# Kernel optimization log

Hardware: AMD Instinct MI355X
Metric: run time of the kernel (lower is better)

Reference implementation:

```python
import jax, jax.numpy as jnp
import numpy as np

MODE = 'max'  # matches init kwarg `mode`
EPS = 1e-6

def before_after(x):
    n, d = x.shape
    zero = jnp.zeros((1, d), dtype=x.dtype)
    if MODE == 'max':
        # exclusive prefix max (x_before[0] = 0, matching torch.zeros_like base)
        pre = jax.lax.cummax(x, axis=0)
        before = jnp.concatenate([zero, pre[:-1]], axis=0)
        suf = jax.lax.cummax(x[::-1], axis=0)[::-1]
        after = jnp.concatenate([suf[1:], zero], axis=0)
    else:  # mean
        cs = jnp.cumsum(x, axis=0)
        cnt_b = jnp.arange(1, n, dtype=x.dtype)[:, None]
        before = jnp.concatenate([zero, cs[:-1] / cnt_b], axis=0)
        total = cs[-1]
        cnt_a = jnp.arange(n - 1, 0, -1, dtype=x.dtype)[:, None]
        after = jnp.concatenate([(total[None, :] - cs[:-1]) / cnt_a, zero], axis=0)
    return before, after

def setup_inputs() -> dict:
    key = jax.random.key(0)
    ks = jax.random.split(key, 6)
    n, dim, dff = 8192, 1024, 4096
    s1 = 1.0 / np.sqrt(3 * dim)
    s2 = 1.0 / np.sqrt(dff)
    return {
        'x': jax.random.normal(ks[0], (n, dim), jnp.float32),
        'W1': jax.random.normal(ks[1], (dff, 3 * dim), jnp.float32) * s1,
        'b1': jax.random.normal(ks[2], (dff,), jnp.float32) * s1,
        'ln_w': jnp.ones((dff,), jnp.float32),
        'ln_b': jnp.zeros((dff,), jnp.float32),
        'W2': jax.random.normal(ks[3], (dim, dff), jnp.float32) * s2,
        'b2': jax.random.normal(ks[4], (dim,), jnp.float32) * s2,
        'gamma': jnp.full((dim,), 1e-6, jnp.float32),
    }

def reference(x, W1, b1, ln_w, ln_b, W2, b2, gamma):
    shortcut = x
    before, after = before_after(x)
    h = jnp.concatenate([x, before, after], axis=1)          # [n, 3*dim]
    h = jax.nn.relu(h @ W1.T + b1)                           # [n, dff]
    mu = jnp.mean(h, axis=-1, keepdims=True)
    var = jnp.mean(jnp.square(h - mu), axis=-1, keepdims=True)
    h = (h - mu) * jax.lax.rsqrt(var + EPS) * ln_w + ln_b
    # dropout is identity in eval mode
    out = h @ W2.T + b2                                      # [n, dim]
    return out * gamma[None, :] + shortcut
```

## Files before the change

kernel.cpp:

```cpp
#include <hip/hip_runtime.h>

typedef __attribute__((ext_vector_type(4))) float f32x4;
typedef __attribute__((ext_vector_type(8))) short s16x8;
typedef __attribute__((ext_vector_type(8))) unsigned short u16x8;

#define AS1(p) ((const __attribute__((address_space(1))) void*)(p))
#define AS3(p) ((__attribute__((address_space(3))) void*)(p))

__device__ __forceinline__ unsigned short f2bf(float f) {
  unsigned u = __builtin_bit_cast(unsigned, f);
  u += 0x7fffu + ((u >> 16) & 1u);
  return (unsigned short)(u >> 16);
}
__device__ __forceinline__ float bf2f(unsigned short s) {
  unsigned u = ((unsigned)s) << 16;
  return __builtin_bit_cast(float, u);
}
__device__ __forceinline__ unsigned f2e4m3(float f) {
  unsigned uf = __builtin_bit_cast(unsigned, f);
  unsigned s = (uf >> 24) & 0x80u;
  unsigned u = uf & 0x7fffffffu;
  if (u < 0x3c800000u) return s;
  if (u > 0x43e00000u) u = 0x43e00000u;
  u += 0x7ffffu + ((u >> 20) & 1u);
  unsigned v = (u >> 20) - 960u;
  if (v > 126u) v = 126u;
  return s | v;
}


__global__ __launch_bounds__(256) void cast_weights(const float* __restrict__ W1,
                                                    unsigned char* __restrict__ W1q,
                                                    long n1,
                                                    const float* __restrict__ W2,
                                                    unsigned short* __restrict__ W2b,
                                                    long n2) {
  if (blockIdx.x < 1536) {
    long i = ((long)blockIdx.x * 256 + threadIdx.x) * 4;
    long stride = (long)1536 * 256 * 4;
    for (; i < n1; i += stride) {
      float4 f = *(const float4*)(W1 + i);
      unsigned v = f2e4m3(f.x * 32.f) | (f2e4m3(f.y * 32.f) << 8) |
                   (f2e4m3(f.z * 32.f) << 16) | (f2e4m3(f.w * 32.f) << 24);
      long n = i / 3072;
      long k = i - n * 3072;
      long phys = n * 3072 + (k & ~(long)127) + ((k & 127) ^ ((n & 15) << 3));
      *(unsigned*)(W1q + phys) = v;
    }
  } else {
    long i = ((long)(blockIdx.x - 1536) * 256 + threadIdx.x) * 4;
    long stride = (long)512 * 256 * 4;
    for (; i < n2; i += stride) {
      float4 f = *(const float4*)(W2 + i);
      ushort4 o = { f2bf(f.x), f2bf(f.y), f2bf(f.z), f2bf(f.w) };
      *(ushort4*)(W2b + i) = o;
    }
  }
}

__global__ __launch_bounds__(256) void w2_fold(const float* __restrict__ W2,
                                               const float* __restrict__ lnw,
                                               const float* __restrict__ lnb,
                                               float* __restrict__ w2l,
                                               float* __restrict__ b2l) {
  const int n = blockIdx.x;
  const float* w = W2 + (long)n * 4096;
  float s = 0.f, b = 0.f;
  for (int k = threadIdx.x; k < 4096; k += 256) {
    float wv = w[k];
    s += wv * lnw[k];
    b += wv * lnb[k];
  }
#pragma unroll
  for (int off = 32; off; off >>= 1) {
    s += __shfl_xor(s, off, 64);
    b += __shfl_xor(b, off, 64);
  }
  __shared__ float ss[4], bb[4];
  const int wv2 = threadIdx.x >> 6;
  if ((threadIdx.x & 63) == 0) { ss[wv2] = s; bb[wv2] = b; }
  __syncthreads();
  if (threadIdx.x == 0) {
    w2l[n] = ss[0] + ss[1] + ss[2] + ss[3];
    b2l[n] = bb[0] + bb[1] + bb[2] + bb[3];
  }
}

__global__ __launch_bounds__(256) void scan_chunkmax(const float* __restrict__ x,
                                                     float* __restrict__ partial) {
  int col = blockIdx.x * 256 + threadIdx.x;
  int chunk = blockIdx.y;
  const float* p = x + (long)chunk * 64 * 1024 + col;
  float m = -INFINITY;
#pragma unroll 4
  for (int i = 0; i < 64; i++) m = fmaxf(m, p[(long)i * 1024]);
  partial[chunk * 1024 + col] = m;
}

__global__ __launch_bounds__(256) void scan_chunkscan(const float* __restrict__ partial,
                                                      float* __restrict__ prefix,
                                                      float* __restrict__ suffix) {
  int col = blockIdx.x * 256 + threadIdx.x;
  float v[128];
#pragma unroll
  for (int c = 0; c < 128; c++) v[c] = partial[c * 1024 + col];
  float run = -INFINITY;
#pragma unroll
  for (int c = 0; c < 128; c++) {
    prefix[c * 1024 + col] = run;
    run = fmaxf(run, v[c]);
  }
  run = -INFINITY;
#pragma unroll
  for (int c = 127; c >= 0; c--) {
    suffix[c * 1024 + col] = run;
    run = fmaxf(run, v[c]);
  }
}

__global__ __launch_bounds__(256) void scan_emit(const float* __restrict__ x,
                                                 const float* __restrict__ prefix,
                                                 const float* __restrict__ suffix,
                                                 unsigned char* __restrict__ h_in) {
  int col = blockIdx.x * 256 + threadIdx.x;
  int chunk = blockIdx.y;
  long r0 = (long)chunk * 64;
  const int cb = col & ~127, cw = col & 127;
  float run = prefix[chunk * 1024 + col];
  for (int i = 0; i < 64; i++) {
    long row = r0 + i;
    int xo = (int)(row & 15) << 3;
    int c0 = cb | (cw ^ xo);
    float v = x[row * 1024 + col];
    unsigned char* hr = h_in + row * 3072;
    hr[c0] = (unsigned char)f2e4m3(v);
    hr[1024 + c0] = (unsigned char)(row == 0 ? 0u : f2e4m3(run));
    run = fmaxf(run, v);
  }
  float run2 = suffix[chunk * 1024 + col];
  for (int i = 63; i >= 0; i--) {
    long row = r0 + i;
    int xo = (int)(row & 15) << 3;
    int c0 = cb | (cw ^ xo);
    float v = x[row * 1024 + col];
    h_in[row * 3072 + 2048 + c0] = (unsigned char)(row == 8191 ? 0u : f2e4m3(run2));
    run2 = fmaxf(run2, v);
  }
}

__global__ __launch_bounds__(256) void ln_stats_reduce(const float* __restrict__ pp,
                                                       float* __restrict__ rowstats) {
  int row = blockIdx.x * 256 + threadIdx.x;
  int tm = row >> 8, rl = row & 255;
  float s = 0.f, q = 0.f;
#pragma unroll
  for (int tn = 0; tn < 16; ++tn) {
    const float* p = pp + (((long)(tm * 16 + tn) * 256 + rl) * 2);
    s += p[0];
    q += p[1];
  }
  float mu = s * (1.f / 4096.f);
  float var = q * (1.f / 4096.f) - mu * mu;
  rowstats[row * 2] = mu;
  rowstats[row * 2 + 1] = rsqrtf(var + 1e-6f);
}

__global__ __launch_bounds__(512, 2) void gemm256_relu(
    const unsigned char* __restrict__ A, const unsigned char* __restrict__ B,
    unsigned short* __restrict__ C, const float* __restrict__ bias,
    const float* __restrict__ lnw, float* __restrict__ pp,
    int M, int N, int K) {
  extern __shared__ char smem[];
  const int NT = K >> 7;

  const int nwg = gridDim.x;
  const int cpx = nwg >> 3;
  const int bid = blockIdx.x;
  const int swz = (bid & 7) * cpx + (bid >> 3);
  const int tiles_m = M >> 8;
  const int tm = swz % tiles_m;
  const int tn = swz / tiles_m;
  const long brow = (long)tm * 256;
  const long bcol = (long)tn * 256;

  const int t = threadIdx.x;
  const int lane = t & 63, wv = t >> 6;
  const int wr = wv >> 2, wc = wv & 3;
  const int fr = lane & 15, fk = lane >> 4;

  const int srow = t >> 3;
  const int scol = (t & 7) * 16;
  const unsigned char* Asrc = A + (brow + srow) * (long)K + scol;
  const unsigned char* Bsrc = B + (bcol + srow) * (long)K + scol;
  const long hstep = (long)128 * K, lstep = (long)64 * K;

#define STAGE_A(j, reg, h, L)                                                   \
  __builtin_amdgcn_global_load_lds(AS1(Asrc + (h)*hstep + (L)*lstep + (j)*128), \
      AS3(smem + (reg)*32768 + (h)*16384 + (L)*8192 + t * 16), 16, 0, 0)
#define STAGE_B(j, h, L)                                                        \
  __builtin_amdgcn_global_load_lds(AS1(Bsrc + (h)*hstep + (L)*lstep + (j)*128), \
      AS3(smem + 98304 + ((j)&1) * 32768 + (h)*16384 + (L)*8192 + t * 16), 16, 0, 0)

  const int xr = fr << 3;
  const char* ArdRow = smem + (wr * 128 + fr) * 128;
  const char* BrdRow = smem + 98304 + (wc * 64 + fr) * 128;
#define RD_A(ar_, m, kk) \
  (*(const long*)(ArdRow + (ar_)*32768 + (m)*2048 + (((kk)*32 + fk * 8) ^ xr)))
#define RD_B(pb_, n, kk) \
  (*(const long*)(BrdRow + (pb_)*32768 + (n)*2048 + (((kk)*32 + fk * 8) ^ xr)))

#define MFMA_QUAD(mi, a_)                                                      \
  _Pragma("unroll")                                                            \
  for (int n = 0; n < 4; ++n) {                                                \
    _Pragma("unroll")                                                          \
    for (int kk = 0; kk < 4; ++kk)                                             \
      acc[(mi)][n] = __builtin_amdgcn_mfma_f32_16x16x32_fp8_fp8(               \
          a_[kk], bfr[n][kk], acc[(mi)][n], 0, 0, 0);                          \
  }

  f32x4 acc[8][4];
#pragma unroll
  for (int m = 0; m < 8; m++)
#pragma unroll
    for (int n = 0; n < 4; n++) acc[m][n] = (f32x4)0.f;

  STAGE_A(0, 0, 0, 0); STAGE_A(0, 0, 0, 1); STAGE_A(0, 0, 1, 0); STAGE_A(0, 0, 1, 1);
  STAGE_B(0, 0, 0); STAGE_B(0, 0, 1); STAGE_B(0, 1, 0); STAGE_B(0, 1, 1);
  STAGE_A(1, 1, 0, 0); STAGE_A(1, 1, 0, 1); STAGE_A(1, 1, 1, 0); STAGE_A(1, 1, 1, 1);
  STAGE_B(1, 0, 0); STAGE_B(1, 0, 1); STAGE_B(1, 1, 0); STAGE_B(1, 1, 1);
  asm volatile("s_waitcnt vmcnt(8)" ::: "memory");
  __builtin_amdgcn_s_barrier();

  long bfr[4][4];
  long ap[2][2][4];
  ap[0][0][0] = RD_A(0, 0, 0); ap[0][0][1] = RD_A(0, 0, 1);
  ap[0][0][2] = RD_A(0, 0, 2); ap[0][0][3] = RD_A(0, 0, 3);
  ap[0][1][0] = RD_A(0, 1, 0); ap[0][1][1] = RD_A(0, 1, 1);
  ap[0][1][2] = RD_A(0, 1, 2); ap[0][1][3] = RD_A(0, 1, 3);

  int ar = 0;
  for (int g = 0; g < NT; ++g) {
    const int pb = g & 1;
    int sr = ar + 2; if (sr >= 3) sr -= 3;
    int nar = ar + 1; if (nar >= 3) nar = 0;
    const bool st = (g + 2 < NT);
#pragma unroll
    for (int p = 0; p < 4; ++p) {
      const int cs = p & 1, ns = cs ^ 1;
      if (p == 0) {
#pragma unroll
        for (int n = 0; n < 4; ++n)
#pragma unroll
          for (int kk = 0; kk < 4; ++kk) bfr[n][kk] = RD_B(pb, n, kk);
      }
      asm volatile("s_waitcnt lgkmcnt(0)" ::: "memory");
      __builtin_amdgcn_sched_barrier(0);
      __builtin_amdgcn_s_setprio(1);
      MFMA_QUAD(2 * p, ap[cs][0])
      MFMA_QUAD(2 * p + 1, ap[cs][1])
      __builtin_amdgcn_s_setprio(0);
      if (p < 3) {
#pragma unroll
        for (int kk = 0; kk < 4; ++kk) {
          ap[ns][0][kk] = RD_A(ar, 2 * p + 2, kk);
          ap[ns][1][kk] = RD_A(ar, 2 * p + 3, kk);
        }
      } else if (g + 1 < NT) {
#pragma unroll
        for (int kk = 0; kk < 4; ++kk) {
          ap[ns][0][kk] = RD_A(nar, 0, kk);
          ap[ns][1][kk] = RD_A(nar, 1, kk);
        }
      }
      if (st) {
        if (p == 0) { STAGE_A(g + 2, sr, 0, 0); STAGE_A(g + 2, sr, 0, 1); }
        if (p == 1) { STAGE_A(g + 2, sr, 1, 0); STAGE_A(g + 2, sr, 1, 1); }
        if (p == 2) { STAGE_B(g + 2, 0, 0); STAGE_B(g + 2, 0, 1); }
        if (p == 3) { STAGE_B(g + 2, 1, 0); STAGE_B(g + 2, 1, 1); }
      }
      if (p == 2 && g + 1 < NT) {
        if (st) asm volatile("s_waitcnt vmcnt(6)" ::: "memory");
        else    asm volatile("s_waitcnt vmcnt(0)" ::: "memory");
      }
      asm volatile("s_barrier" ::: "memory");
    }
    ar = nar;
  }

  float bi[4], lw[4];
#pragma unroll
  for (int n = 0; n < 4; ++n) {
    const long col = bcol + wc * 64 + n * 16 + fr;
    bi[n] = bias[col];
    lw[n] = lnw[col];
  }
  float* sred = (float*)smem;
  float* qred = sred + 1024;
  const long orow = brow + wr * 128 + fk * 4;
  const long ocol = bcol + wc * 64 + fr;
#pragma unroll
  for (int m = 0; m < 8; ++m) {
#pragma unroll
    for (int r = 0; r < 4; ++r) {
      const long row = orow + m * 16 + r;
      float s = 0.f, q = 0.f;
#pragma unroll
      for (int n = 0; n < 4; ++n) {
        float v = acc[m][n][r] * 0.03125f + bi[n];
        v = v > 0.f ? v : 0.f;
        s += v;
        q += v * v;
        C[row * (long)N + ocol + n * 16] = f2bf(v * lw[n]);
      }
#pragma unroll
      for (int off = 1; off < 16; off <<= 1) {
        s += __shfl_xor(s, off, 64);
        q += __shfl_xor(q, off, 64);
      }
      if (fr == 0) {
        int rl = wr * 128 + m * 16 + fk * 4 + r;
        sred[rl * 4 + wc] = s;
        qred[rl * 4 + wc] = q;
      }
    }
  }
  __syncthreads();
  if (t < 256) {
    float s = sred[t * 4] + sred[t * 4 + 1] + sred[t * 4 + 2] + sred[t * 4 + 3];
    float q = qred[t * 4] + qred[t * 4 + 1] + qred[t * 4 + 2] + qred[t * 4 + 3];
    float* pb = pp + (((long)(tm * 16 + tn) * 256 + t) * 2);
    pb[0] = s;
    pb[1] = q;
  }
#undef STAGE_A
#undef STAGE_B
#undef RD_A
#undef RD_B
#undef MFMA_QUAD
}

__global__ __launch_bounds__(512, 2) void gemm256_g2(
    const unsigned short* __restrict__ A, const unsigned short* __restrict__ B,
    float* __restrict__ Cf, const float* __restrict__ bias,
    const float* __restrict__ gamma, const float* __restrict__ resid,
    const float* __restrict__ w2l, const float* __restrict__ b2l,
    const float* __restrict__ rowstats,
    int M, int N, int K) {
  extern __shared__ char smem[];
  const int NT = K >> 6;

  const int nwg = gridDim.x;
  const int cpx = nwg >> 3;
  const int bid = blockIdx.x;
  const int swz = (bid & 7) * cpx + (bid >> 3);
  const int tiles_m = M >> 8;
  const int tm = swz % tiles_m;
  const int tn = swz / tiles_m;
  const long brow = (long)tm * 256;
  const long bcol = (long)tn * 128;

  const int t = threadIdx.x;
  const int lane = t & 63, wv = t >> 6;
  const int wr = wv >> 1, wc = wv & 1;
  const int fr = lane & 15, fk = lane >> 4;

  const int srow = t >> 3;
  const int scol = 8 * ((t & 7) ^ ((t >> 3) & 7));
  const unsigned short* Asrc = A + (brow + srow) * (long)K + scol;
  const unsigned short* Bsrc = B + (bcol + srow) * (long)K + scol;
  const long hstep = (long)128 * K, lstep = (long)64 * K;

#define STAGE_A2(j, reg, h, L)                                                 \
  __builtin_amdgcn_global_load_lds(AS1(Asrc + (h)*hstep + (L)*lstep + (j)*64), \
      AS3(smem + (reg)*32768 + (h)*16384 + (L)*8192 + t * 16), 16, 0, 0)
#define STAGE_B2(j, L)                                                         \
  __builtin_amdgcn_global_load_lds(AS1(Bsrc + (L)*lstep + (j)*64),             \
      AS3(smem + 98304 + ((j)&1) * 16384 + (L)*8192 + t * 16), 16, 0, 0)

  const int xr = (fr & 7) << 4;
  const char* ArdRow = smem + (wr * 64 + fr) * 128;
  const char* BrdRow = smem + 98304 + (wc * 64 + fr) * 128;
#define RD_A2(ar_, m, kk) \
  (*(const s16x8*)(ArdRow + (ar_)*32768 + (m)*2048 + (((kk)*64 + fk * 16) ^ xr)))
#define RD_B2(pb_, n, kk) \
  (*(const s16x8*)(BrdRow + (pb_)*16384 + (n)*2048 + (((kk)*64 + fk * 16) ^ xr)))

  f32x4 acc[4][4];
#pragma unroll
  for (int m = 0; m < 4; m++)
#pragma unroll
    for (int n = 0; n < 4; n++) acc[m][n] = (f32x4)0.f;

  STAGE_A2(0, 0, 0, 0); STAGE_A2(0, 0, 0, 1); STAGE_A2(0, 0, 1, 0); STAGE_A2(0, 0, 1, 1);
  STAGE_B2(0, 0); STAGE_B2(0, 1);
  STAGE_A2(1, 1, 0, 0); STAGE_A2(1, 1, 0, 1); STAGE_A2(1, 1, 1, 0); STAGE_A2(1, 1, 1, 1);
  STAGE_B2(1, 0); STAGE_B2(1, 1);
  asm volatile("s_waitcnt vmcnt(6)" ::: "memory");
  __builtin_amdgcn_s_barrier();

  s16x8 bfr[4][2];
  s16x8 ap[2][2];
  ap[0][0] = RD_A2(0, 0, 0); ap[0][1] = RD_A2(0, 0, 1);

  int ar = 0;
  for (int g = 0; g < NT; ++g) {
    const int pb = g & 1;
    int sr = ar + 2; if (sr >= 3) sr -= 3;
    int nar = ar + 1; if (nar >= 3) nar = 0;
    const bool st = (g + 2 < NT);
#pragma unroll
    for (int p = 0; p < 4; ++p) {
      const int cs = p & 1, ns = cs ^ 1;
      if (p == 0) {
#pragma unroll
        for (int n = 0; n < 4; ++n) {
          bfr[n][0] = RD_B2(pb, n, 0);
          bfr[n][1] = RD_B2(pb, n, 1);
        }
      }
      asm volatile("s_waitcnt lgkmcnt(0)" ::: "memory");
      __builtin_amdgcn_sched_barrier(0);
      __builtin_amdgcn_s_setprio(1);
#pragma unroll
      for (int n = 0; n < 4; ++n) {
        acc[p][n] = __builtin_amdgcn_mfma_f32_16x16x32_bf16(
            ap[cs][0], bfr[n][0], acc[p][n], 0, 0, 0);
        acc[p][n] = __builtin_amdgcn_mfma_f32_16x16x32_bf16(
            ap[cs][1], bfr[n][1], acc[p][n], 0, 0, 0);
      }
      __builtin_amdgcn_s_setprio(0);
      if (p < 3) {
        ap[ns][0] = RD_A2(ar, p + 1, 0); ap[ns][1] = RD_A2(ar, p + 1, 1);
      } else if (g + 1 < NT) {
        ap[ns][0] = RD_A2(nar, 0, 0); ap[ns][1] = RD_A2(nar, 0, 1);
      }
      if (st) {
        if (p == 0) { STAGE_A2(g + 2, sr, 0, 0); STAGE_A2(g + 2, sr, 0, 1); }
        if (p == 1) { STAGE_A2(g + 2, sr, 1, 0); STAGE_A2(g + 2, sr, 1, 1); }
        if (p == 2) { STAGE_B2(g + 2, 0); STAGE_B2(g + 2, 1); }
      }
      if (p == 2 && g + 1 < NT) {
        if (st) asm volatile("s_waitcnt vmcnt(6)" ::: "memory");
        else    asm volatile("s_waitcnt vmcnt(0)" ::: "memory");
      }
      asm volatile("s_barrier" ::: "memory");
    }
    ar = nar;
  }

  float bi[4], ga[4], wl[4], bl[4];
#pragma unroll
  for (int n = 0; n < 4; ++n) {
    const long col = bcol + wc * 64 + n * 16 + fr;
    bi[n] = bias[col];
    ga[n] = gamma[col];
    wl[n] = w2l[col];
    bl[n] = b2l[col];
  }
  const long orow = brow + wr * 64 + fk * 4;
  const long ocol = bcol + wc * 64 + fr;
#pragma unroll
  for (int m = 0; m < 4; ++m)
#pragma unroll
    for (int r = 0; r < 4; ++r) {
      const long row = orow + m * 16 + r;
      const float mu = rowstats[row * 2];
      const float rs = rowstats[row * 2 + 1];
#pragma unroll
      for (int n = 0; n < 4; ++n) {
        const long col = ocol + n * 16;
        float v = rs * acc[m][n][r] - rs * mu * wl[n] + bl[n] + bi[n];
        Cf[row * (long)N + col] = v * ga[n] + resid[row * (long)N + col];
      }
    }
#undef STAGE_A2
#undef STAGE_B2
#undef RD_A2
#undef RD_B2
}

extern "C" void kernel_launch(void* const* d_in, const int* in_sizes, int n_in,
                              void* d_out, int out_size, void* d_ws, size_t ws_size,
                              hipStream_t stream) {
  const float* x     = (const float*)d_in[0];
  const float* W1    = (const float*)d_in[1];
  const float* b1    = (const float*)d_in[2];
  const float* ln_w  = (const float*)d_in[3];
  const float* ln_b  = (const float*)d_in[4];
  const float* W2    = (const float*)d_in[5];
  const float* b2    = (const float*)d_in[6];
  const float* gamma = (const float*)d_in[7];
  float* out = (float*)d_out;

  const int Nr = 8192, DIM = 1024, DFF = 4096, K1 = 3072;

  unsigned char* W1q    = (unsigned char*)d_ws;
  unsigned short* W2b   = (unsigned short*)(W1q + (long)DFF * K1);
  unsigned char* h_in   = (unsigned char*)(W2b + (long)DIM * DFF);
  unsigned short* h_act = (unsigned short*)(h_in + (long)Nr * K1);
  float* partial  = (float*)(h_act + (long)Nr * DFF);
  float* prefix   = partial + 128 * 1024;
  float* suffix   = prefix + 128 * 1024;
  float* pp       = suffix + 128 * 1024;
  float* rowstats = pp + 32 * 16 * 256 * 2;
  float* w2l      = rowstats + (long)Nr * 2;
  float* b2l      = w2l + DIM;

  hipFuncSetAttribute((const void*)gemm256_relu,
                      hipFuncAttributeMaxDynamicSharedMemorySize, 163840);
  hipFuncSetAttribute((const void*)gemm256_g2,
                      hipFuncAttributeMaxDynamicSharedMemorySize, 131072);

  cast_weights<<<2048, 256, 0, stream>>>(W1, W1q, (long)DFF * K1,
                                         W2, W2b, (long)DIM * DFF);

  scan_chunkmax<<<dim3(4, 128), 256, 0, stream>>>(x, partial);
  scan_chunkscan<<<4, 256, 0, stream>>>(partial, prefix, suffix);
  scan_emit<<<dim3(4, 128), 256, 0, stream>>>(x, prefix, suffix, h_in);

  w2_fold<<<DIM, 256, 0, stream>>>(W2, ln_w, ln_b, w2l, b2l);

  gemm256_relu<<<512, 512, 163840, stream>>>(h_in, W1q, h_act, b1, ln_w, pp,
                                             Nr, DFF, K1);

  ln_stats_reduce<<<32, 256, 0, stream>>>(pp, rowstats);

  gemm256_g2<<<256, 512, 131072, stream>>>(h_act, W2b, out, b2, gamma, x,
                                           w2l, b2l, rowstats, Nr, DIM, DFF);
}
```

Before: 315.0 us.

## Switch second GEMM to FP8 operands with swizzled e4m3 activations and weights

Quantizes W2 and the post-ReLU hidden activations to e4m3 (scaled by 32, stored in the same XOR-swizzled layout as W1q) instead of bf16. The second GEMM now loads K=128 byte tiles and uses fp8 MFMA, rescaling accumulators by 1/32. This halves the memory traffic of the hidden activation buffer and of W2, and uses the higher fp8 MFMA throughput. The cost is lower precision in the second matmul, and the activation store in the first GEMM becomes byte-granular scattered writes.

New measurement: 297.2 us. 5.7% less time.

```diff
diff --git a/kernel.cpp b/kernel.cpp
--- a/kernel.cpp
+++ b/kernel.cpp
@@ -33,7 +33,7 @@
                                                     unsigned char* __restrict__ W1q,
                                                     long n1,
                                                     const float* __restrict__ W2,
-                                                    unsigned short* __restrict__ W2b,
+                                                    unsigned char* __restrict__ W2q,
                                                     long n2) {
   if (blockIdx.x < 1536) {
     long i = ((long)blockIdx.x * 256 + threadIdx.x) * 4;
@@ -52,8 +52,12 @@
     long stride = (long)512 * 256 * 4;
     for (; i < n2; i += stride) {
       float4 f = *(const float4*)(W2 + i);
-      ushort4 o = { f2bf(f.x), f2bf(f.y), f2bf(f.z), f2bf(f.w) };
-      *(ushort4*)(W2b + i) = o;
+      unsigned v = f2e4m3(f.x * 32.f) | (f2e4m3(f.y * 32.f) << 8) |
+                   (f2e4m3(f.z * 32.f) << 16) | (f2e4m3(f.w * 32.f) << 24);
+      long n = i >> 12;
+      long k = i & 4095;
+      long phys = (n << 12) + (k & ~(long)127) + ((k & 127) ^ ((n & 15) << 3));
+      *(unsigned*)(W2q + phys) = v;
     }
   }
 }
@@ -167,7 +171,7 @@
 
 __global__ __launch_bounds__(512, 2) void gemm256_relu(
     const unsigned char* __restrict__ A, const unsigned char* __restrict__ B,
-    unsigned short* __restrict__ C, const float* __restrict__ bias,
+    unsigned char* __restrict__ C, const float* __restrict__ bias,
     const float* __restrict__ lnw, float* __restrict__ pp,
     int M, int N, int K) {
   extern __shared__ char smem[];
@@ -297,12 +301,13 @@
   float* sred = (float*)smem;
   float* qred = sred + 1024;
   const long orow = brow + wr * 128 + fk * 4;
-  const long ocol = bcol + wc * 64 + fr;
+  const int ocol = (int)bcol + wc * 64 + fr;
 #pragma unroll
   for (int m = 0; m < 8; ++m) {
 #pragma unroll
     for (int r = 0; r < 4; ++r) {
       const long row = orow + m * 16 + r;
+      const int xo = ((fk * 4 + r) & 15) << 3;
       float s = 0.f, q = 0.f;
 #pragma unroll
       for (int n = 0; n < 4; ++n) {
@@ -310,7 +315,9 @@
         v = v > 0.f ? v : 0.f;
         s += v;
         q += v * v;
-        C[row * (long)N + ocol + n * 16] = f2bf(v * lw[n]);
+        const int col = ocol + n * 16;
+        const int phys = (col & ~127) | ((col & 127) ^ xo);
+        C[row * (long)N + phys] = (unsigned char)f2e4m3(v * lw[n]);
       }
 #pragma unroll
       for (int off = 1; off < 16; off <<= 1) {
@@ -340,14 +347,14 @@
 }
 
 __global__ __launch_bounds__(512, 2) void gemm256_g2(
-    const unsigned short* __restrict__ A, const unsigned short* __restrict__ B,
+    const unsigned char* __restrict__ A, const unsigned char* __restrict__ B,
     float* __restrict__ Cf, const float* __restrict__ bias,
     const float* __restrict__ gamma, const float* __restrict__ resid,
     const float* __restrict__ w2l, const float* __restrict__ b2l,
     const float* __restrict__ rowstats,
     int M, int N, int K) {
   extern __shared__ char smem[];
-  const int NT = K >> 6;
+  const int NT = K >> 7;
 
   const int nwg = gridDim.x;
   const int cpx = nwg >> 3;
@@ -365,25 +372,25 @@
   const int fr = lane & 15, fk = lane >> 4;
 
   const int srow = t >> 3;
-  const int scol = 8 * ((t & 7) ^ ((t >> 3) & 7));
-  const unsigned short* Asrc = A + (brow + srow) * (long)K + scol;
-  const unsigned short* Bsrc = B + (bcol + srow) * (long)K + scol;
+  const int scol = (t & 7) * 16;
+  const unsigned char* Asrc = A + (brow + srow) * (long)K + scol;
+  const unsigned char* Bsrc = B + (bcol + srow) * (long)K + scol;
   const long hstep = (long)128 * K, lstep = (long)64 * K;
 
-#define STAGE_A2(j, reg, h, L)                                                 \
-  __builtin_amdgcn_global_load_lds(AS1(Asrc + (h)*hstep + (L)*lstep + (j)*64), \
+#define STAGE_A2(j, reg, h, L)                                                  \
+  __builtin_amdgcn_global_load_lds(AS1(Asrc + (h)*hstep + (L)*lstep + (j)*128), \
       AS3(smem + (reg)*32768 + (h)*16384 + (L)*8192 + t * 16), 16, 0, 0)
-#define STAGE_B2(j, L)                                                         \
-  __builtin_amdgcn_global_load_lds(AS1(Bsrc + (L)*lstep + (j)*64),             \
+#define STAGE_B2(j, L)                                                          \
+  __builtin_amdgcn_global_load_lds(AS1(Bsrc + (L)*lstep + (j)*128),             \
       AS3(smem + 98304 + ((j)&1) * 16384 + (L)*8192 + t * 16), 16, 0, 0)
 
-  const int xr = (fr & 7) << 4;
+  const int xr = fr << 3;
   const char* ArdRow = smem + (wr * 64 + fr) * 128;
   const char* BrdRow = smem + 98304 + (wc * 64 + fr) * 128;
 #define RD_A2(ar_, m, kk) \
-  (*(const s16x8*)(ArdRow + (ar_)*32768 + (m)*2048 + (((kk)*64 + fk * 16) ^ xr)))
+  (*(const long*)(ArdRow + (ar_)*32768 + (m)*2048 + (((kk)*32 + fk * 8) ^ xr)))
 #define RD_B2(pb_, n, kk) \
-  (*(const s16x8*)(BrdRow + (pb_)*16384 + (n)*2048 + (((kk)*64 + fk * 16) ^ xr)))
+  (*(const long*)(BrdRow + (pb_)*16384 + (n)*2048 + (((kk)*32 + fk * 8) ^ xr)))
 
   f32x4 acc[4][4];
 #pragma unroll
@@ -398,9 +405,10 @@
   asm volatile("s_waitcnt vmcnt(6)" ::: "memory");
   __builtin_amdgcn_s_barrier();
 
-  s16x8 bfr[4][2];
-  s16x8 ap[2][2];
+  long bfr[4][4];
+  long ap[2][4];
   ap[0][0] = RD_A2(0, 0, 0); ap[0][1] = RD_A2(0, 0, 1);
+  ap[0][2] = RD_A2(0, 0, 2); ap[0][3] = RD_A2(0, 0, 3);
 
   int ar = 0;
   for (int g = 0; g < NT; ++g) {
@@ -413,26 +421,26 @@
       const int cs = p & 1, ns = cs ^ 1;
       if (p == 0) {
 #pragma unroll
-        for (int n = 0; n < 4; ++n) {
-          bfr[n][0] = RD_B2(pb, n, 0);
-          bfr[n][1] = RD_B2(pb, n, 1);
-        }
+        for (int n = 0; n < 4; ++n)
+#pragma unroll
+          for (int kk = 0; kk < 4; ++kk) bfr[n][kk] = RD_B2(pb, n, kk);
       }
       asm volatile("s_waitcnt lgkmcnt(0)" ::: "memory");
       __builtin_amdgcn_sched_barrier(0);
       __builtin_amdgcn_s_setprio(1);
 #pragma unroll
-      for (int n = 0; n < 4; ++n) {
-        acc[p][n] = __builtin_amdgcn_mfma_f32_16x16x32_bf16(
-            ap[cs][0], bfr[n][0], acc[p][n], 0, 0, 0);
-        acc[p][n] = __builtin_amdgcn_mfma_f32_16x16x32_bf16(
-            ap[cs][1], bfr[n][1], acc[p][n], 0, 0, 0);
-      }
+      for (int n = 0; n < 4; ++n)
+#pragma unroll
+        for (int kk = 0; kk < 4; ++kk)
+          acc[p][n] = __builtin_amdgcn_mfma_f32_16x16x32_fp8_fp8(
+              ap[cs][kk], bfr[n][kk], acc[p][n], 0, 0, 0);
       __builtin_amdgcn_s_setprio(0);
       if (p < 3) {
-        ap[ns][0] = RD_A2(ar, p + 1, 0); ap[ns][1] = RD_A2(ar, p + 1, 1);
+#pragma unroll
+        for (int kk = 0; kk < 4; ++kk) ap[ns][kk] = RD_A2(ar, p + 1, kk);
       } else if (g + 1 < NT) {
-        ap[ns][0] = RD_A2(nar, 0, 0); ap[ns][1] = RD_A2(nar, 0, 1);
+#pragma unroll
+        for (int kk = 0; kk < 4; ++kk) ap[ns][kk] = RD_A2(nar, 0, kk);
       }
       if (st) {
         if (p == 0) { STAGE_A2(g + 2, sr, 0, 0); STAGE_A2(g + 2, sr, 0, 1); }
@@ -469,7 +477,7 @@
 #pragma unroll
       for (int n = 0; n < 4; ++n) {
         const long col = ocol + n * 16;
-        float v = rs * acc[m][n][r] - rs * mu * wl[n] + bl[n] + bi[n];
+        float v = rs * (acc[m][n][r] * 0.03125f) - rs * mu * wl[n] + bl[n] + bi[n];
         Cf[row * (long)N + col] = v * ga[n] + resid[row * (long)N + col];
       }
     }
@@ -494,10 +502,10 @@
 
   const int Nr = 8192, DIM = 1024, DFF = 4096, K1 = 3072;
 
-  unsigned char* W1q    = (unsigned char*)d_ws;
-  unsigned short* W2b   = (unsigned short*)(W1q + (long)DFF * K1);
-  unsigned char* h_in   = (unsigned char*)(W2b + (long)DIM * DFF);
-  unsigned short* h_act = (unsigned short*)(h_in + (long)Nr * K1);
+  unsigned char* W1q   = (unsigned char*)d_ws;
+  unsigned char* W2q   = W1q + (long)DFF * K1;
+  unsigned char* h_in  = W2q + (long)DIM * DFF;
+  unsigned char* h_act = h_in + (long)Nr * K1;
   float* partial  = (float*)(h_act + (long)Nr * DFF);
   float* prefix   = partial + 128 * 1024;
   float* suffix   = prefix + 128 * 1024;
@@ -512,7 +520,7 @@
                       hipFuncAttributeMaxDynamicSharedMemorySize, 131072);
 
   cast_weights<<<2048, 256, 0, stream>>>(W1, W1q, (long)DFF * K1,
-                                         W2, W2b, (long)DIM * DFF);
+                                         W2, W2q, (long)DIM * DFF);
 
   scan_chunkmax<<<dim3(4, 128), 256, 0, stream>>>(x, partial);
   scan_chunkscan<<<4, 256, 0, stream>>>(partial, prefix, suffix);
@@ -525,6 +533,6 @@
 
   ln_stats_reduce<<<32, 256, 0, stream>>>(pp, rowstats);
 
-  gemm256_g2<<<256, 512, 131072, stream>>>(h_act, W2b, out, b2, gamma, x,
+  gemm256_g2<<<256, 512, 131072, stream>>>(h_act, W2q, out, b2, gamma, x,
                                            w2l, b2l, rowstats, Nr, DIM, DFF);
 }
```
